# Kernel optimization log

Measured on AMD Instinct MI355X. Metric: run time of the kernel, lower is better.

Reference implementation:

```python
import jax, jax.numpy as jnp
import numpy as np

LX = LY = KS = 14            # lengthX, lengthY, kernel_size
IN_BOND = 4
HID = 4                      # hidden_bond
CH = 2                       # channel
OUT = 10                     # output_dim
N = 32768                    # batch
LENGTH = LX * LY             # 196 sequential contraction steps
P = (LX - KS + 1) * (LY - KS + 1)  # number of patches (=1 here)
STD = 0.01
EPS = 1e-5                   # BatchNorm1d default eps


def setup_inputs() -> dict:
    key = jax.random.key(0)
    k0, k1, k2, k3 = jax.random.split(key, 4)
    x = jax.random.normal(k0, (N, IN_BOND, LX, LY), jnp.float32)
    # weights1[0]: [in_bond, hidden, channel]
    w_first = STD * jax.random.normal(k1, (IN_BOND, HID, CH), jnp.float32)
    # weights1[1..length-2]: [hidden, in_bond, hidden, channel], stacked
    w_mid = STD * jax.random.normal(k2, (LENGTH - 2, HID, IN_BOND, HID, CH), jnp.float32)
    # weights1[length-1]: [hidden, in_bond, output_dim, channel]
    w_last = STD * jax.random.normal(k3, (HID, IN_BOND, OUT, CH), jnp.float32)
    # shared BatchNorm1d(hidden) affine params
    gamma = jnp.ones((HID,), jnp.float32)
    beta = jnp.zeros((HID,), jnp.float32)
    return {"x": x, "w_first": w_first, "w_mid": w_mid, "w_last": w_last,
            "gamma": gamma, "beta": beta}


def reference(x, w_first, w_mid, w_last, gamma, beta):
    n = x.shape[0]
    # Patch extraction -> InputBucket [N, in_bond, KS*KS, P]
    buckets = []
    for k in range(LX - KS + 1):          # static, size 1 with defaults
        for l in range(LY - KS + 1):
            buckets.append(x[:, :, k:k + KS, l:l + KS].reshape(n, IN_BOND, KS * KS))
    ib = jnp.stack(buckets, axis=3)       # [N, in_bond, KS*KS, P]

    # Step 0: tensordot over in_bond, then permute -> y 'nbcr' = [N, P, CH, HID]
    y = jnp.einsum('nip,ihc->npch', ib[:, :, 0, :], w_first)

    # Middle steps 1..LENGTH-2 as a scan (strict sequential dependency chain)
    mids = jnp.moveaxis(ib[:, :, 1:LENGTH - 1, :], 2, 0)  # [LENGTH-2, N, in_bond, P]

    def step(y, inp):
        xi, w = inp  # xi: [N, in_bond, P]; w: [HID(r), IN_BOND(i), HID(h), CH(c)]
        # contra_w_d after permute: [N, P, CH, HID_left(r), HID_right(h)]
        contra = jnp.einsum('nip,rihc->npcrh', xi, w)
        y_new = jnp.einsum('npcr,npcrh->ncph', y, contra)  # 'ncbl': [N, CH, P, HID]
        # BatchNorm1d(HID) in training mode over flattened batch (biased var)
        flat = y_new.reshape(-1, HID)
        mean = jnp.mean(flat, axis=0)
        var = jnp.var(flat, axis=0)
        yb = (flat - mean) * jax.lax.rsqrt(var + EPS) * gamma + beta
        # faithful to torch's .view(-1, P, CH, HID) memory reinterpretation
        return yb.reshape(n, P, CH, HID), None

    y, _ = jax.lax.scan(step, y, (mids, w_mid))

    # Last step: -> [N, P, CH, HID, OUT] then einsum 'nbcr,nbcrl->nbcl'
    contra = jnp.einsum('nip,rioc->npcro', ib[:, :, LENGTH - 1, :], w_last)
    out = jnp.einsum('npcr,npcro->npco', y, contra)  # [N, P, CH, OUT]
    return out
```

## Files before the change

kernel.cpp:

```cpp
#include <hip/hip_runtime.h>

#define NSAMP 32768
#define INB   4
#define HIDN  4
#define CHN   2
#define OUTD  10
#define NPIX  196
#define NMID  194
#define BLK   256
#define SPT   2
#define NBLK  (NSAMP / (BLK * SPT))
#define INV_ROWS 1.52587890625e-05f
#define BN_EPS 1e-5f
#define SENT  0xFFFFFFFFFFFFFFFFull
#define WS_BYTES ((size_t)NMID * NBLK * 4 * sizeof(unsigned long long))

__device__ __forceinline__ float xcomp(const float4& v, int j) {
    return j == 0 ? v.x : j == 1 ? v.y : j == 2 ? v.z : v.w;
}

__device__ __forceinline__ void mid_step(
    int t, const float xv[SPT][INB], float y[SPT][CHN][HIDN],
    const float* __restrict__ wm,
    const float gm[HIDN], const float bt[HIDN],
    unsigned long long* __restrict__ slots, float (*pb)[8], int tid)
{
    const float* w = wm + (long)t * (HIDN * INB * HIDN * CHN);
    float yn[SPT][CHN][HIDN];
#pragma unroll
    for (int s = 0; s < SPT; ++s)
#pragma unroll
        for (int c = 0; c < CHN; ++c)
#pragma unroll
            for (int h = 0; h < HIDN; ++h) yn[s][c][h] = 0.f;

#pragma unroll
    for (int s = 0; s < SPT; ++s)
#pragma unroll
        for (int r = 0; r < HIDN; ++r)
#pragma unroll
            for (int i = 0; i < INB; ++i) {
                float p0 = y[s][0][r] * xv[s][i];
                float p1 = y[s][1][r] * xv[s][i];
                const float* wri = w + r * (INB * HIDN * CHN) + i * (HIDN * CHN);
#pragma unroll
                for (int h = 0; h < HIDN; ++h) {
                    yn[s][0][h] = fmaf(p0, wri[h * CHN + 0], yn[s][0][h]);
                    yn[s][1][h] = fmaf(p1, wri[h * CHN + 1], yn[s][1][h]);
                }
            }
    float red[8];
#pragma unroll
    for (int h = 0; h < HIDN; ++h) {
        float sm = 0.f, sq = 0.f;
#pragma unroll
        for (int s = 0; s < SPT; ++s) {
            sm += yn[s][0][h] + yn[s][1][h];
            sq += yn[s][0][h] * yn[s][0][h] + yn[s][1][h] * yn[s][1][h];
        }
        red[h] = sm; red[4 + h] = sq;
    }
#pragma unroll
    for (int j = 0; j < 8; ++j)
#pragma unroll
        for (int off = 32; off > 0; off >>= 1)
            red[j] += __shfl_down(red[j], off);
    const int wv = tid >> 6, ln = tid & 63;
    if (ln == 0) {
#pragma unroll
        for (int j = 0; j < 8; ++j) pb[wv][j] = red[j];
    }
    __syncthreads();
    if (tid < 4) {
        float lo = pb[0][2 * tid]     + pb[1][2 * tid]     + pb[2][2 * tid]     + pb[3][2 * tid];
        float hi = pb[0][2 * tid + 1] + pb[1][2 * tid + 1] + pb[2][2 * tid + 1] + pb[3][2 * tid + 1];
        unsigned long long v = ((unsigned long long)__float_as_uint(hi) << 32)
                             |  (unsigned long long)__float_as_uint(lo);
        __hip_atomic_store(&slots[((size_t)t * NBLK + blockIdx.x) * 4 + tid], v,
                           __ATOMIC_RELAXED, __HIP_MEMORY_SCOPE_AGENT);
    }
    const unsigned long long* ps = &slots[((size_t)t * NBLK + ln) * 4];
    unsigned long long q0, q1, q2, q3;
    do {
        q0 = __hip_atomic_load(&ps[0], __ATOMIC_RELAXED, __HIP_MEMORY_SCOPE_AGENT);
        q1 = __hip_atomic_load(&ps[1], __ATOMIC_RELAXED, __HIP_MEMORY_SCOPE_AGENT);
        q2 = __hip_atomic_load(&ps[2], __ATOMIC_RELAXED, __HIP_MEMORY_SCOPE_AGENT);
        q3 = __hip_atomic_load(&ps[3], __ATOMIC_RELAXED, __HIP_MEMORY_SCOPE_AGENT);
    } while (!__all(q0 != SENT && q1 != SENT && q2 != SENT && q3 != SENT));
    float sm[8];
    sm[0] = __uint_as_float((unsigned)q0); sm[1] = __uint_as_float((unsigned)(q0 >> 32));
    sm[2] = __uint_as_float((unsigned)q1); sm[3] = __uint_as_float((unsigned)(q1 >> 32));
    sm[4] = __uint_as_float((unsigned)q2); sm[5] = __uint_as_float((unsigned)(q2 >> 32));
    sm[6] = __uint_as_float((unsigned)q3); sm[7] = __uint_as_float((unsigned)(q3 >> 32));
#pragma unroll
    for (int j = 0; j < 8; ++j)
#pragma unroll
        for (int off = 1; off < 64; off <<= 1)
            sm[j] += __shfl_xor(sm[j], off);
#pragma unroll
    for (int h = 0; h < HIDN; ++h) {
        float m  = sm[h] * INV_ROWS;
        float v  = fmaf(-m, m, sm[4 + h] * INV_ROWS);
        float is = rsqrtf(v + BN_EPS) * gm[h];
        float sh = bt[h] - m * is;
#pragma unroll
        for (int s = 0; s < SPT; ++s) {
            y[s][0][h] = fmaf(yn[s][0][h], is, sh);
            y[s][1][h] = fmaf(yn[s][1][h], is, sh);
        }
    }
}

__global__ __launch_bounds__(BLK, 1)
void ttbn_main(const float* __restrict__ x,  const float* __restrict__ wf,
               const float* __restrict__ wm, const float* __restrict__ wl,
               const float* __restrict__ gamma, const float* __restrict__ beta,
               float* __restrict__ out, unsigned long long* __restrict__ slots)
{
    __shared__ float pb[BLK / 64][8];
    const int tid = threadIdx.x;

    float gm[HIDN], bt[HIDN];
#pragma unroll
    for (int h = 0; h < HIDN; ++h) { gm[h] = gamma[h]; bt[h] = beta[h]; }

    const float* xn[SPT];
    long nidx[SPT];
#pragma unroll
    for (int s = 0; s < SPT; ++s) {
        nidx[s] = (long)blockIdx.x * (BLK * SPT) + s * BLK + tid;
        xn[s]   = x + nidx[s] * (INB * NPIX);
    }

    float4 xg[SPT][INB];
    float  y[SPT][CHN][HIDN];

#pragma unroll
    for (int s = 0; s < SPT; ++s)
#pragma unroll
        for (int i = 0; i < INB; ++i)
            xg[s][i] = *reinterpret_cast<const float4*>(xn[s] + i * NPIX);

#pragma unroll
    for (int s = 0; s < SPT; ++s)
#pragma unroll
        for (int c = 0; c < CHN; ++c)
#pragma unroll
            for (int h = 0; h < HIDN; ++h) {
                float acc = 0.f;
#pragma unroll
                for (int i = 0; i < INB; ++i)
                    acc = fmaf(xg[s][i].x, wf[i * (HIDN * CHN) + h * CHN + c], acc);
                y[s][c][h] = acc;
            }
#pragma unroll
    for (int slp = 1; slp < 4; ++slp) {
        float xv[SPT][INB];
#pragma unroll
        for (int s = 0; s < SPT; ++s)
#pragma unroll
            for (int i = 0; i < INB; ++i) xv[s][i] = xcomp(xg[s][i], slp);
        mid_step(slp - 1, xv, y, wm, gm, bt, slots, pb, tid);
    }

#pragma unroll 1
    for (int g = 1; g < 48; ++g) {
#pragma unroll
        for (int s = 0; s < SPT; ++s)
#pragma unroll
            for (int i = 0; i < INB; ++i)
                xg[s][i] = *reinterpret_cast<const float4*>(xn[s] + i * NPIX + g * 4);
#pragma unroll
        for (int slp = 0; slp < 4; ++slp) {
            float xv[SPT][INB];
#pragma unroll
            for (int s = 0; s < SPT; ++s)
#pragma unroll
                for (int i = 0; i < INB; ++i) xv[s][i] = xcomp(xg[s][i], slp);
            mid_step(g * 4 + slp - 1, xv, y, wm, gm, bt, slots, pb, tid);
        }
    }

#pragma unroll
    for (int s = 0; s < SPT; ++s)
#pragma unroll
        for (int i = 0; i < INB; ++i)
            xg[s][i] = *reinterpret_cast<const float4*>(xn[s] + i * NPIX + 192);
#pragma unroll
    for (int slp = 0; slp < 3; ++slp) {
        float xv[SPT][INB];
#pragma unroll
        for (int s = 0; s < SPT; ++s)
#pragma unroll
            for (int i = 0; i < INB; ++i) xv[s][i] = xcomp(xg[s][i], slp);
        mid_step(191 + slp, xv, y, wm, gm, bt, slots, pb, tid);
    }
#pragma unroll
    for (int s = 0; s < SPT; ++s) {
        float xv[INB];
#pragma unroll
        for (int i = 0; i < INB; ++i) xv[i] = xg[s][i].w;
        float o0[OUTD], o1[OUTD];
#pragma unroll
        for (int od = 0; od < OUTD; ++od) { o0[od] = 0.f; o1[od] = 0.f; }
#pragma unroll
        for (int r = 0; r < HIDN; ++r)
#pragma unroll
            for (int i = 0; i < INB; ++i) {
                float p0 = y[s][0][r] * xv[i];
                float p1 = y[s][1][r] * xv[i];
                const float* wri = wl + r * (INB * OUTD * CHN) + i * (OUTD * CHN);
#pragma unroll
                for (int od = 0; od < OUTD; ++od) {
                    o0[od] = fmaf(p0, wri[od * CHN + 0], o0[od]);
                    o1[od] = fmaf(p1, wri[od * CHN + 1], o1[od]);
                }
            }
        float tmp[20];
#pragma unroll
        for (int od = 0; od < OUTD; ++od) { tmp[od] = o0[od]; tmp[10 + od] = o1[od]; }
        float4* o4 = reinterpret_cast<float4*>(out + nidx[s] * (CHN * OUTD));
#pragma unroll
        for (int q = 0; q < 5; ++q)
            o4[q] = make_float4(tmp[q * 4], tmp[q * 4 + 1], tmp[q * 4 + 2], tmp[q * 4 + 3]);
    }
}

extern "C" void kernel_launch(void* const* d_in, const int* in_sizes, int n_in,
                              void* d_out, int out_size, void* d_ws, size_t ws_size,
                              hipStream_t stream) {
    const float* x     = (const float*)d_in[0];
    const float* wf    = (const float*)d_in[1];
    const float* wm    = (const float*)d_in[2];
    const float* wl    = (const float*)d_in[3];
    const float* gamma = (const float*)d_in[4];
    const float* beta  = (const float*)d_in[5];
    float*       out   = (float*)d_out;
    unsigned long long* slots = (unsigned long long*)d_ws;

    hipMemsetAsync(d_ws, 0xFF, WS_BYTES, stream);

    void* args[] = { &x, &wf, &wm, &wl, &gamma, &beta, &out, &slots };
    hipLaunchCooperativeKernel((void*)ttbn_main, dim3(NBLK), dim3(BLK),
                               args, 0, stream);
}
```

Measured before the change: 936.8 us.

## Precompute next step's contraction matrix while waiting on grid-wide BN reduction

Each thread now owns one sample with 512-thread blocks. Per step it first contracts x with w into a per-sample 2x4x4 matrix M, then applies M to y. The M for the next step is computed between publishing this block's partial sums and spinning on the other blocks' slots, so that work sits inside the barrier latency. Only wave 0 polls the global slots and passes the totals through shared memory, which costs an extra __syncthreads per step. The number of blocks participating in the grid-wide reduction is unchanged.

```diff
diff --git a/kernel.cpp b/kernel.cpp
--- a/kernel.cpp
+++ b/kernel.cpp
@@ -7,9 +7,8 @@
 #define OUTD  10
 #define NPIX  196
 #define NMID  194
-#define BLK   256
-#define SPT   2
-#define NBLK  (NSAMP / (BLK * SPT))
+#define BLK   512
+#define NBLK  (NSAMP / BLK)
 #define INV_ROWS 1.52587890625e-05f
 #define BN_EPS 1e-5f
 #define SENT  0xFFFFFFFFFFFFFFFFull
@@ -17,98 +16,6 @@
 
 __device__ __forceinline__ float xcomp(const float4& v, int j) {
     return j == 0 ? v.x : j == 1 ? v.y : j == 2 ? v.z : v.w;
-}
-
-__device__ __forceinline__ void mid_step(
-    int t, const float xv[SPT][INB], float y[SPT][CHN][HIDN],
-    const float* __restrict__ wm,
-    const float gm[HIDN], const float bt[HIDN],
-    unsigned long long* __restrict__ slots, float (*pb)[8], int tid)
-{
-    const float* w = wm + (long)t * (HIDN * INB * HIDN * CHN);
-    float yn[SPT][CHN][HIDN];
-#pragma unroll
-    for (int s = 0; s < SPT; ++s)
-#pragma unroll
-        for (int c = 0; c < CHN; ++c)
-#pragma unroll
-            for (int h = 0; h < HIDN; ++h) yn[s][c][h] = 0.f;
-
-#pragma unroll
-    for (int s = 0; s < SPT; ++s)
-#pragma unroll
-        for (int r = 0; r < HIDN; ++r)
-#pragma unroll
-            for (int i = 0; i < INB; ++i) {
-                float p0 = y[s][0][r] * xv[s][i];
-                float p1 = y[s][1][r] * xv[s][i];
-                const float* wri = w + r * (INB * HIDN * CHN) + i * (HIDN * CHN);
-#pragma unroll
-                for (int h = 0; h < HIDN; ++h) {
-                    yn[s][0][h] = fmaf(p0, wri[h * CHN + 0], yn[s][0][h]);
-                    yn[s][1][h] = fmaf(p1, wri[h * CHN + 1], yn[s][1][h]);
-                }
-            }
-    float red[8];
-#pragma unroll
-    for (int h = 0; h < HIDN; ++h) {
-        float sm = 0.f, sq = 0.f;
-#pragma unroll
-        for (int s = 0; s < SPT; ++s) {
-            sm += yn[s][0][h] + yn[s][1][h];
-            sq += yn[s][0][h] * yn[s][0][h] + yn[s][1][h] * yn[s][1][h];
-        }
-        red[h] = sm; red[4 + h] = sq;
-    }
-#pragma unroll
-    for (int j = 0; j < 8; ++j)
-#pragma unroll
-        for (int off = 32; off > 0; off >>= 1)
-            red[j] += __shfl_down(red[j], off);
-    const int wv = tid >> 6, ln = tid & 63;
-    if (ln == 0) {
-#pragma unroll
-        for (int j = 0; j < 8; ++j) pb[wv][j] = red[j];
-    }
-    __syncthreads();
-    if (tid < 4) {
-        float lo = pb[0][2 * tid]     + pb[1][2 * tid]     + pb[2][2 * tid]     + pb[3][2 * tid];
-        float hi = pb[0][2 * tid + 1] + pb[1][2 * tid + 1] + pb[2][2 * tid + 1] + pb[3][2 * tid + 1];
-        unsigned long long v = ((unsigned long long)__float_as_uint(hi) << 32)
-                             |  (unsigned long long)__float_as_uint(lo);
-        __hip_atomic_store(&slots[((size_t)t * NBLK + blockIdx.x) * 4 + tid], v,
-                           __ATOMIC_RELAXED, __HIP_MEMORY_SCOPE_AGENT);
-    }
-    const unsigned long long* ps = &slots[((size_t)t * NBLK + ln) * 4];
-    unsigned long long q0, q1, q2, q3;
-    do {
-        q0 = __hip_atomic_load(&ps[0], __ATOMIC_RELAXED, __HIP_MEMORY_SCOPE_AGENT);
-        q1 = __hip_atomic_load(&ps[1], __ATOMIC_RELAXED, __HIP_MEMORY_SCOPE_AGENT);
-        q2 = __hip_atomic_load(&ps[2], __ATOMIC_RELAXED, __HIP_MEMORY_SCOPE_AGENT);
-        q3 = __hip_atomic_load(&ps[3], __ATOMIC_RELAXED, __HIP_MEMORY_SCOPE_AGENT);
-    } while (!__all(q0 != SENT && q1 != SENT && q2 != SENT && q3 != SENT));
-    float sm[8];
-    sm[0] = __uint_as_float((unsigned)q0); sm[1] = __uint_as_float((unsigned)(q0 >> 32));
-    sm[2] = __uint_as_float((unsigned)q1); sm[3] = __uint_as_float((unsigned)(q1 >> 32));
-    sm[4] = __uint_as_float((unsigned)q2); sm[5] = __uint_as_float((unsigned)(q2 >> 32));
-    sm[6] = __uint_as_float((unsigned)q3); sm[7] = __uint_as_float((unsigned)(q3 >> 32));
-#pragma unroll
-    for (int j = 0; j < 8; ++j)
-#pragma unroll
-        for (int off = 1; off < 64; off <<= 1)
-            sm[j] += __shfl_xor(sm[j], off);
-#pragma unroll
-    for (int h = 0; h < HIDN; ++h) {
-        float m  = sm[h] * INV_ROWS;
-        float v  = fmaf(-m, m, sm[4 + h] * INV_ROWS);
-        float is = rsqrtf(v + BN_EPS) * gm[h];
-        float sh = bt[h] - m * is;
-#pragma unroll
-        for (int s = 0; s < SPT; ++s) {
-            y[s][0][h] = fmaf(yn[s][0][h], is, sh);
-            y[s][1][h] = fmaf(yn[s][1][h], is, sh);
-        }
-    }
 }
 
 __global__ __launch_bounds__(BLK, 1)
@@ -118,88 +25,153 @@
                float* __restrict__ out, unsigned long long* __restrict__ slots)
 {
     __shared__ float pb[BLK / 64][8];
+    __shared__ float totl[8];
     const int tid = threadIdx.x;
+    const int ln  = tid & 63, wv = tid >> 6;
+    const long n  = (long)blockIdx.x * BLK + tid;
 
     float gm[HIDN], bt[HIDN];
 #pragma unroll
     for (int h = 0; h < HIDN; ++h) { gm[h] = gamma[h]; bt[h] = beta[h]; }
 
-    const float* xn[SPT];
-    long nidx[SPT];
-#pragma unroll
-    for (int s = 0; s < SPT; ++s) {
-        nidx[s] = (long)blockIdx.x * (BLK * SPT) + s * BLK + tid;
-        xn[s]   = x + nidx[s] * (INB * NPIX);
-    }
-
-    float4 xg[SPT][INB];
-    float  y[SPT][CHN][HIDN];
-
-#pragma unroll
-    for (int s = 0; s < SPT; ++s)
-#pragma unroll
-        for (int i = 0; i < INB; ++i)
-            xg[s][i] = *reinterpret_cast<const float4*>(xn[s] + i * NPIX);
-
-#pragma unroll
-    for (int s = 0; s < SPT; ++s)
+    const float* xrow = x + n * (INB * NPIX);
+
+    float4 xq[INB];
+#pragma unroll
+    for (int i = 0; i < INB; ++i)
+        xq[i] = *reinterpret_cast<const float4*>(xrow + i * NPIX);
+
+    float y[CHN][HIDN];
+#pragma unroll
+    for (int c = 0; c < CHN; ++c)
+#pragma unroll
+        for (int h = 0; h < HIDN; ++h) {
+            float acc = 0.f;
+#pragma unroll
+            for (int i = 0; i < INB; ++i)
+                acc = fmaf(xq[i].x, wf[i * (HIDN * CHN) + h * CHN + c], acc);
+            y[c][h] = acc;
+        }
+    float M[CHN][HIDN][HIDN];
+#pragma unroll
+    for (int c = 0; c < CHN; ++c)
+#pragma unroll
+        for (int r = 0; r < HIDN; ++r)
+#pragma unroll
+            for (int h = 0; h < HIDN; ++h) {
+                float m = 0.f;
+#pragma unroll
+                for (int i = 0; i < INB; ++i)
+                    m = fmaf(xq[i].y, wm[(r * 16 + i * 4 + h) * 2 + c], m);
+                M[c][r][h] = m;
+            }
+
+    float yn[CHN][HIDN];
+
+#pragma unroll 1
+    for (int t = 0; t < NMID; ++t) {
 #pragma unroll
         for (int c = 0; c < CHN; ++c)
 #pragma unroll
             for (int h = 0; h < HIDN; ++h) {
                 float acc = 0.f;
 #pragma unroll
+                for (int r = 0; r < HIDN; ++r)
+                    acc = fmaf(y[c][r], M[c][r][h], acc);
+                yn[c][h] = acc;
+            }
+        float red[8];
+#pragma unroll
+        for (int h = 0; h < HIDN; ++h) {
+            red[h]     = yn[0][h] + yn[1][h];
+            red[4 + h] = yn[0][h] * yn[0][h] + yn[1][h] * yn[1][h];
+        }
+#pragma unroll
+        for (int j = 0; j < 8; ++j)
+#pragma unroll
+            for (int off = 32; off > 0; off >>= 1)
+                red[j] += __shfl_down(red[j], off);
+        if (ln == 0) {
+#pragma unroll
+            for (int j = 0; j < 8; ++j) pb[wv][j] = red[j];
+        }
+        __syncthreads();
+        if (wv == 0 && ln < 4) {
+            float lo = 0.f, hi = 0.f;
+#pragma unroll
+            for (int w = 0; w < 8; ++w) {
+                lo += pb[w][2 * ln];
+                hi += pb[w][2 * ln + 1];
+            }
+            unsigned long long v = ((unsigned long long)__float_as_uint(hi) << 32)
+                                 |  (unsigned long long)__float_as_uint(lo);
+            __hip_atomic_store(&slots[((size_t)t * NBLK + blockIdx.x) * 4 + ln], v,
+                               __ATOMIC_RELAXED, __HIP_MEMORY_SCOPE_AGENT);
+        }
+        if (t < NMID - 1) {
+            const int q = t + 2;
+            if ((q & 3) == 0) {
+#pragma unroll
                 for (int i = 0; i < INB; ++i)
-                    acc = fmaf(xg[s][i].x, wf[i * (HIDN * CHN) + h * CHN + c], acc);
-                y[s][c][h] = acc;
-            }
-#pragma unroll
-    for (int slp = 1; slp < 4; ++slp) {
-        float xv[SPT][INB];
-#pragma unroll
-        for (int s = 0; s < SPT; ++s)
-#pragma unroll
-            for (int i = 0; i < INB; ++i) xv[s][i] = xcomp(xg[s][i], slp);
-        mid_step(slp - 1, xv, y, wm, gm, bt, slots, pb, tid);
+                    xq[i] = *reinterpret_cast<const float4*>(xrow + i * NPIX + q);
+            }
+            float xv[INB];
+#pragma unroll
+            for (int i = 0; i < INB; ++i) xv[i] = xcomp(xq[i], q & 3);
+            const float* w1 = wm + (size_t)(t + 1) * 128;
+#pragma unroll
+            for (int c = 0; c < CHN; ++c)
+#pragma unroll
+                for (int r = 0; r < HIDN; ++r)
+#pragma unroll
+                    for (int h = 0; h < HIDN; ++h) {
+                        float m = 0.f;
+#pragma unroll
+                        for (int i = 0; i < INB; ++i)
+                            m = fmaf(xv[i], w1[(r * 16 + i * 4 + h) * 2 + c], m);
+                        M[c][r][h] = m;
+                    }
+        }
+        if (wv == 0) {
+            const unsigned long long* ps = &slots[((size_t)t * NBLK + ln) * 4];
+            unsigned long long q0, q1, q2, q3;
+            do {
+                q0 = __hip_atomic_load(&ps[0], __ATOMIC_RELAXED, __HIP_MEMORY_SCOPE_AGENT);
+                q1 = __hip_atomic_load(&ps[1], __ATOMIC_RELAXED, __HIP_MEMORY_SCOPE_AGENT);
+                q2 = __hip_atomic_load(&ps[2], __ATOMIC_RELAXED, __HIP_MEMORY_SCOPE_AGENT);
+                q3 = __hip_atomic_load(&ps[3], __ATOMIC_RELAXED, __HIP_MEMORY_SCOPE_AGENT);
+            } while (!__all(q0 != SENT && q1 != SENT && q2 != SENT && q3 != SENT));
+            float sm[8];
+            sm[0] = __uint_as_float((unsigned)q0); sm[1] = __uint_as_float((unsigned)(q0 >> 32));
+            sm[2] = __uint_as_float((unsigned)q1); sm[3] = __uint_as_float((unsigned)(q1 >> 32));
+            sm[4] = __uint_as_float((unsigned)q2); sm[5] = __uint_as_float((unsigned)(q2 >> 32));
+            sm[6] = __uint_as_float((unsigned)q3); sm[7] = __uint_as_float((unsigned)(q3 >> 32));
+#pragma unroll
+            for (int j = 0; j < 8; ++j)
+#pragma unroll
+                for (int off = 1; off < 64; off <<= 1)
+                    sm[j] += __shfl_xor(sm[j], off);
+            if (ln < 8) totl[ln] = sm[ln];
+        }
+        __syncthreads();
+        float s0 = totl[0], s1 = totl[1], s2 = totl[2], s3 = totl[3];
+        float t0 = totl[4], t1 = totl[5], t2 = totl[6], t3 = totl[7];
+        float smv[8] = {s0, s1, s2, s3, t0, t1, t2, t3};
+#pragma unroll
+        for (int h = 0; h < HIDN; ++h) {
+            float m  = smv[h] * INV_ROWS;
+            float v  = fmaf(-m, m, smv[4 + h] * INV_ROWS);
+            float is = rsqrtf(v + BN_EPS) * gm[h];
+            float sh = bt[h] - m * is;
+            y[0][h] = fmaf(yn[0][h], is, sh);
+            y[1][h] = fmaf(yn[1][h], is, sh);
+        }
     }
 
-#pragma unroll 1
-    for (int g = 1; g < 48; ++g) {
-#pragma unroll
-        for (int s = 0; s < SPT; ++s)
-#pragma unroll
-            for (int i = 0; i < INB; ++i)
-                xg[s][i] = *reinterpret_cast<const float4*>(xn[s] + i * NPIX + g * 4);
-#pragma unroll
-        for (int slp = 0; slp < 4; ++slp) {
-            float xv[SPT][INB];
-#pragma unroll
-            for (int s = 0; s < SPT; ++s)
-#pragma unroll
-                for (int i = 0; i < INB; ++i) xv[s][i] = xcomp(xg[s][i], slp);
-            mid_step(g * 4 + slp - 1, xv, y, wm, gm, bt, slots, pb, tid);
-        }
-    }
-
-#pragma unroll
-    for (int s = 0; s < SPT; ++s)
-#pragma unroll
-        for (int i = 0; i < INB; ++i)
-            xg[s][i] = *reinterpret_cast<const float4*>(xn[s] + i * NPIX + 192);
-#pragma unroll
-    for (int slp = 0; slp < 3; ++slp) {
-        float xv[SPT][INB];
-#pragma unroll
-        for (int s = 0; s < SPT; ++s)
-#pragma unroll
-            for (int i = 0; i < INB; ++i) xv[s][i] = xcomp(xg[s][i], slp);
-        mid_step(191 + slp, xv, y, wm, gm, bt, slots, pb, tid);
-    }
-#pragma unroll
-    for (int s = 0; s < SPT; ++s) {
+    {
         float xv[INB];
 #pragma unroll
-        for (int i = 0; i < INB; ++i) xv[i] = xg[s][i].w;
+        for (int i = 0; i < INB; ++i) xv[i] = xq[i].w;
         float o0[OUTD], o1[OUTD];
 #pragma unroll
         for (int od = 0; od < OUTD; ++od) { o0[od] = 0.f; o1[od] = 0.f; }
@@ -207,8 +179,8 @@
         for (int r = 0; r < HIDN; ++r)
 #pragma unroll
             for (int i = 0; i < INB; ++i) {
-                float p0 = y[s][0][r] * xv[i];
-                float p1 = y[s][1][r] * xv[i];
+                float p0 = y[0][r] * xv[i];
+                float p1 = y[1][r] * xv[i];
                 const float* wri = wl + r * (INB * OUTD * CHN) + i * (OUTD * CHN);
 #pragma unroll
                 for (int od = 0; od < OUTD; ++od) {
@@ -219,7 +191,7 @@
         float tmp[20];
 #pragma unroll
         for (int od = 0; od < OUTD; ++od) { tmp[od] = o0[od]; tmp[10 + od] = o1[od]; }
-        float4* o4 = reinterpret_cast<float4*>(out + nidx[s] * (CHN * OUTD));
+        float4* o4 = reinterpret_cast<float4*>(out + n * (CHN * OUTD));
 #pragma unroll
         for (int q = 0; q < 5; ++q)
             o4[q] = make_float4(tmp[q * 4], tmp[q * 4 + 1], tmp[q * 4 + 2], tmp[q * 4 + 3]);
```

Measured after the change: 795.5 us. 15.1% less time.
